# Kernel tuning notes

Hardware: AMD Instinct MI355X
Metric: run time of the kernel (lower is better)

## Reference

```python
import jax, jax.numpy as jnp
import numpy as np

B, L, D_MODEL = 2, 1024, 512
D_INNER, D_STATE, DT_RANK, D_CONV = 1024, 16, 32, 4
N_LAYER, VOCAB, EMBED_DIM, NUM_EMOTIONS = 2, 30000, 256, 7


def setup_inputs() -> dict:
    key = jax.random.key(0)
    ks = jax.random.split(key, 12)
    def n(k, shape, scale=0.02):
        return jax.random.normal(k, shape, jnp.float32) * scale
    A_init = jnp.broadcast_to(jnp.arange(1, D_STATE + 1, dtype=jnp.float32), (N_LAYER, D_INNER, D_STATE))
    return {
        "input_ids": jax.random.randint(ks[0], (B, L), 0, VOCAB),
        "embedding": n(ks[1], (VOCAB, D_MODEL)),
        "norm_w": jnp.ones((N_LAYER, D_MODEL)),
        "in_proj_w": n(ks[2], (N_LAYER, D_MODEL, 2 * D_INNER)),
        "conv_w": n(ks[3], (N_LAYER, D_INNER, 1, D_CONV), 0.1),
        "conv_b": jnp.zeros((N_LAYER, D_INNER)),
        "x_proj_w": n(ks[4], (N_LAYER, D_INNER, DT_RANK + 2 * D_STATE)),
        "dt_proj_w": n(ks[5], (N_LAYER, DT_RANK, D_INNER), 0.1),
        "dt_proj_b": jnp.zeros((N_LAYER, D_INNER)),
        "A_log": jnp.log(A_init),
        "D": jnp.ones((N_LAYER, D_INNER)),
        "out_proj_w": n(ks[6], (N_LAYER, D_INNER, D_MODEL)),
        "norm_f_w": jnp.ones((D_MODEL,)),
        "proj_w": n(ks[7], (D_MODEL, EMBED_DIM)),
        "proj_b": jnp.zeros((EMBED_DIM,)),
        "cls_w": n(ks[8], (EMBED_DIM, NUM_EMOTIONS)),
        "cls_b": jnp.zeros((NUM_EMOTIONS,)),
    }


def rmsnorm(x, w, eps=1e-5):
    return x * jax.lax.rsqrt(jnp.mean(x * x, axis=-1, keepdims=True) + eps) * w


def selective_scan(u, delta, A, B_, C, D_):
    # u, delta: [b,l,d]; A: [d,n]; B_, C: [b,l,n]; D_: [d]
    dA = jnp.exp(jnp.einsum('bld,dn->bldn', delta, A))          # [b,l,d,n]
    dBu = jnp.einsum('bld,bln,bld->bldn', delta, B_, u)          # [b,l,d,n]
    def step(h, inp):
        dA_t, dBu_t, C_t = inp                                   # [b,d,n],[b,d,n],[b,n]
        h = dA_t * h + dBu_t
        y = jnp.einsum('bdn,bn->bd', h, C_t)
        return h, y
    h0 = jnp.zeros((u.shape[0], u.shape[2], A.shape[1]), u.dtype)
    _, ys = jax.lax.scan(step, h0, (dA.transpose(1, 0, 2, 3), dBu.transpose(1, 0, 2, 3), C.transpose(1, 0, 2)))
    return ys.transpose(1, 0, 2) + u * D_                        # [b,l,d]


def mamba_block(x, in_w, cw, cb, xp_w, dt_w, dt_b, A_log, D_, out_w):
    # x: [b,l,d_model]
    xr = x @ in_w                                                # [b,l,2*d_inner]
    xi, res = jnp.split(xr, 2, axis=-1)
    # causal depthwise conv1d over time
    xc = jax.lax.conv_general_dilated(
        xi.transpose(0, 2, 1), cw, window_strides=(1,),
        padding=[(D_CONV - 1, 0)], feature_group_count=D_INNER,
        dimension_numbers=('NCH', 'OIH', 'NCH'))
    xi = jax.nn.silu(xc.transpose(0, 2, 1) + cb)                 # [b,l,d_inner]
    x_dbl = xi @ xp_w
    delta, B_, C = jnp.split(x_dbl, [DT_RANK, DT_RANK + D_STATE], axis=-1)
    delta = jax.nn.softplus(delta @ dt_w + dt_b)                 # [b,l,d_inner]
    A = -jnp.exp(A_log)
    y = selective_scan(xi, delta, A, B_, C, D_)
    y = y * jax.nn.silu(res)
    return y @ out_w                                             # [b,l,d_model]


def reference(input_ids, embedding, norm_w, in_proj_w, conv_w, conv_b, x_proj_w,
              dt_proj_w, dt_proj_b, A_log, D, out_proj_w, norm_f_w,
              proj_w, proj_b, cls_w, cls_b):
    x = embedding[input_ids]                                     # [b,l,d_model]
    for i in range(N_LAYER):
        x = x + mamba_block(rmsnorm(x, norm_w[i]), in_proj_w[i], conv_w[i],
                            conv_b[i], x_proj_w[i], dt_proj_w[i], dt_proj_b[i],
                            A_log[i], D[i], out_proj_w[i])
    x = rmsnorm(x, norm_f_w)
    pooled = x.mean(axis=1)                                      # [b,d_model]
    emotion_emb = pooled @ proj_w + proj_b                       # [b,embed_dim]
    logits = emotion_emb @ cls_w + cls_b                         # [b,num_emotions]
    return logits, emotion_emb
```

## Files before the change

kernel.cpp:

```cpp
#include <hip/hip_runtime.h>
#include <cstddef>

#define D_MODEL   512
#define D_INNER   1024
#define D_STATE   16
#define DT_RANK   32
#define SEQ_L     1024
#define BATCH     2
#define NLAYER    2
#define M_ROWS    (BATCH * SEQ_L)
#define NC        64
#define LC        (SEQ_L / NC)

typedef __bf16 bf16x8 __attribute__((ext_vector_type(8)));
typedef float  f32x4  __attribute__((ext_vector_type(4)));

__device__ __forceinline__ float softplus_f(float x) {
    return fmaxf(x, 0.f) + log1pf(expf(-fabsf(x)));
}
__device__ __forceinline__ float silu_f(float x) {
    return x / (1.f + __expf(-x));
}
__device__ __forceinline__ unsigned short f2bf(float f) {
    unsigned u = __float_as_uint(f);
    return (unsigned short)((u + 0x7fffu + ((u >> 16) & 1u)) >> 16);
}
__device__ __forceinline__ float bf2f(unsigned short v) {
    return __uint_as_float(((unsigned)v) << 16);
}
__device__ __forceinline__ unsigned pack_bf2(float lo, float hi) {
    return (unsigned)f2bf(lo) | ((unsigned)f2bf(hi) << 16);
}

__global__ __launch_bounds__(256) void init_kernel(const int* __restrict__ ids,
                                                   const float* __restrict__ emb,
                                                   const float* __restrict__ in_w,
                                                   const float* __restrict__ out_w,
                                                   float* __restrict__ x,
                                                   unsigned short* __restrict__ in_wt_all,
                                                   unsigned short* __restrict__ out_wt_all) {
    int z = blockIdx.z;
    if (z == 4) {
        int blk = blockIdx.y * 64 + blockIdx.x;
        if (blk >= 1024) return;
        int g = blk * 256 + threadIdx.x;
        int c = (g & 127) << 2;
        int m = g >> 7;
        int row = ids[m];
        *(float4*)&x[(size_t)m * D_MODEL + c] =
            *(const float4*)&emb[(size_t)row * D_MODEL + c];
        return;
    }
    const float* W; unsigned short* Wt; int K, N;
    if (z < 2) {
        if (blockIdx.x >= 64 || blockIdx.y >= 16) return;
        W = in_w + (size_t)z * 512 * 2048; Wt = in_wt_all + (size_t)z * 2048 * 512;
        K = 512; N = 2048;
    } else {
        int zz = z - 2;
        if (blockIdx.x >= 16 || blockIdx.y >= 32) return;
        W = out_w + (size_t)zz * 1024 * 512; Wt = out_wt_all + (size_t)zz * 512 * 1024;
        K = 1024; N = 512;
    }
    __shared__ float tile[32][33];
    int n0 = blockIdx.x * 32, k0 = blockIdx.y * 32;
    int tx = threadIdx.x & 31, ty = threadIdx.x >> 5;
    #pragma unroll
    for (int i = 0; i < 4; ++i)
        tile[ty + i*8][tx] = W[(size_t)(k0 + ty + i*8) * N + n0 + tx];
    __syncthreads();
    #pragma unroll
    for (int i = 0; i < 4; ++i)
        Wt[(size_t)(n0 + ty + i*8) * K + k0 + tx] = f2bf(tile[tx][ty + i*8]);
}

__global__ __launch_bounds__(64) void rmsnorm_bf_kernel(const float* __restrict__ x,
                                                        const float* __restrict__ w,
                                                        unsigned short* __restrict__ out) {
    int row = blockIdx.x;
    int tid = threadIdx.x;
    const float* xp = x + (size_t)row * D_MODEL;
    float4 v0 = *(const float4*)&xp[tid * 4];
    float4 v1 = *(const float4*)&xp[256 + tid * 4];
    float ss = v0.x*v0.x + v0.y*v0.y + v0.z*v0.z + v0.w*v0.w
             + v1.x*v1.x + v1.y*v1.y + v1.z*v1.z + v1.w*v1.w;
    #pragma unroll
    for (int off = 32; off > 0; off >>= 1) ss += __shfl_xor(ss, off);
    float scale = rsqrtf(ss * (1.f / D_MODEL) + 1e-5f);
    float4 w0 = *(const float4*)&w[tid * 4];
    float4 w1 = *(const float4*)&w[256 + tid * 4];
    unsigned short* op = out + (size_t)row * D_MODEL;
    uint2 p0, p1;
    p0.x = pack_bf2(v0.x * scale * w0.x, v0.y * scale * w0.y);
    p0.y = pack_bf2(v0.z * scale * w0.z, v0.w * scale * w0.w);
    p1.x = pack_bf2(v1.x * scale * w1.x, v1.y * scale * w1.y);
    p1.y = pack_bf2(v1.z * scale * w1.z, v1.w * scale * w1.w);
    *(uint2*)&op[tid * 4] = p0;
    *(uint2*)&op[256 + tid * 4] = p1;
}

template<int BMT, int BNT, int EPI>
__global__ __launch_bounds__(256) void gemm_mfma_t(const unsigned short* __restrict__ A,
                                                   const unsigned short* __restrict__ Bt,
                                                   float* __restrict__ C,
                                                   unsigned short* __restrict__ Cb,
                                                   int K, int ldc) {
    constexpr int FM = BMT / 32;
    constexpr int FN = BNT / 32;
    __shared__ unsigned short As[BMT * 64];
    __shared__ unsigned short Bs[BNT * 64];
    int m0 = blockIdx.y * BMT;
    int n0 = blockIdx.x * BNT;
    int t = threadIdx.x;
    int lane = t & 63, wave = t >> 6;
    int wr = wave >> 1, wc = wave & 1;
    int srow = t >> 3;
    int sc8  = t & 7;
    f32x4 acc[FM][FN] = {};

    for (int k0 = 0; k0 < K; k0 += 64) {
        __syncthreads();
        #pragma unroll
        for (int i = 0; i < BMT / 32; ++i) {
            int row = i * 32 + srow;
            int csrc = sc8 ^ (row & 7);
            __builtin_amdgcn_global_load_lds(
                (const __attribute__((address_space(1))) void*)
                    &A[(size_t)(m0 + row) * K + k0 + csrc * 8],
                (__attribute__((address_space(3))) void*)
                    &As[row * 64 + sc8 * 8], 16, 0, 0);
        }
        #pragma unroll
        for (int i = 0; i < BNT / 32; ++i) {
            int row = i * 32 + srow;
            int csrc = sc8 ^ (row & 7);
            __builtin_amdgcn_global_load_lds(
                (const __attribute__((address_space(1))) void*)
                    &Bt[(size_t)(n0 + row) * K + k0 + csrc * 8],
                (__attribute__((address_space(3))) void*)
                    &Bs[row * 64 + sc8 * 8], 16, 0, 0);
        }
        __syncthreads();
        #pragma unroll
        for (int ks = 0; ks < 2; ++ks) {
            bf16x8 av[FM], bv[FN];
            #pragma unroll
            for (int f = 0; f < FM; ++f) {
                int ar = wr * (FM * 16) + f * 16 + (lane & 15);
                int ac = (ks * 4 + (lane >> 4)) ^ (ar & 7);
                av[f] = *reinterpret_cast<const bf16x8*>(&As[ar * 64 + ac * 8]);
            }
            #pragma unroll
            for (int f = 0; f < FN; ++f) {
                int br = wc * (FN * 16) + f * 16 + (lane & 15);
                int bc = (ks * 4 + (lane >> 4)) ^ (br & 7);
                bv[f] = *reinterpret_cast<const bf16x8*>(&Bs[br * 64 + bc * 8]);
            }
            #pragma unroll
            for (int fm = 0; fm < FM; ++fm)
                #pragma unroll
                for (int fn = 0; fn < FN; ++fn)
                    acc[fm][fn] = __builtin_amdgcn_mfma_f32_16x16x32_bf16(
                        av[fm], bv[fn], acc[fm][fn], 0, 0, 0);
        }
    }
    #pragma unroll
    for (int fm = 0; fm < FM; ++fm)
        #pragma unroll
        for (int fn = 0; fn < FN; ++fn) {
            int row = m0 + wr * (FM * 16) + fm * 16 + (lane >> 4) * 4;
            int col = n0 + wc * (FN * 16) + fn * 16 + (lane & 15);
            #pragma unroll
            for (int r = 0; r < 4; ++r) {
                if (EPI == 2) C[(size_t)(row + r) * ldc + col] += acc[fm][fn][r];
                else          Cb[(size_t)(row + r) * ldc + col] = f2bf(acc[fm][fn][r]);
            }
        }
}

__global__ void conv_bf_kernel(const unsigned short* __restrict__ xi,
                               const float* __restrict__ cw,
                               const float* __restrict__ cb,
                               unsigned short* __restrict__ u) {
    int g = blockIdx.x * blockDim.x + threadIdx.x;
    int d = g & (D_INNER - 1);
    int m = g >> 10;
    int l = m & (SEQ_L - 1);
    float4 w = *(const float4*)&cw[d * 4];
    const unsigned short* col = &xi[(size_t)m * 2048 + d];
    float x3 = bf2f(col[0]);
    float x2 = (l >= 1) ? bf2f(col[-2048]) : 0.f;
    float x1 = (l >= 2) ? bf2f(col[-4096]) : 0.f;
    float x0 = (l >= 3) ? bf2f(col[-6144]) : 0.f;
    u[g] = f2bf(silu_f(cb[d] + w.x*x0 + w.y*x1 + w.z*x2 + w.w*x3));
}

__global__ __launch_bounds__(256) void xproj_kernel(const unsigned short* __restrict__ u,
                                                    const float* __restrict__ Bw,
                                                    float* __restrict__ Cc) {
    __shared__ float Bsh[64][68];
    __shared__ float Ash[4][64];
    int row0 = blockIdx.x * 4;
    int t = threadIdx.x;
    int tr = t >> 6, c = t & 63;
    int kk = t >> 2, cb4 = (t & 3) << 4;
    float acc = 0.f;
    for (int k0 = 0; k0 < 1024; k0 += 64) {
        __syncthreads();
        #pragma unroll
        for (int j = 0; j < 4; ++j) {
            float4 v = *(const float4*)&Bw[(size_t)(k0 + kk) * 64 + cb4 + j * 4];
            *(float4*)&Bsh[kk][cb4 + j * 4] = v;
        }
        Ash[tr][c] = bf2f(u[(size_t)(row0 + tr) * 1024 + k0 + c]);
        __syncthreads();
        #pragma unroll
        for (int k = 0; k < 64; ++k)
            acc = fmaf(Ash[tr][k], Bsh[k][c], acc);
    }
    Cc[(size_t)(row0 + tr) * 64 + c] = acc;
}

#define BM 64
#define BN 64
#define BKK 16
__global__ __launch_bounds__(256) void gemm_dt(const float* __restrict__ A,
                                               const float* __restrict__ Bm,
                                               const float* __restrict__ bias,
                                               float* __restrict__ C,
                                               int lda, int ldb, int ldc) {
    __shared__ float As[BM][BKK + 4];
    __shared__ float Bs[BKK][BN];
    int tid = threadIdx.x;
    int n0 = blockIdx.x * BN;
    int m0 = blockIdx.y * BM;
    int tx4 = (tid & 15) << 2;
    int ty4 = (tid >> 4) << 2;
    int arow = tid >> 2, akk = (tid & 3) << 2;
    int brow = tid >> 4, bcol = (tid & 15) << 2;
    float acc[4][4] = {};
    for (int k0 = 0; k0 < 32; k0 += BKK) {
        float4 av = *(const float4*)&A[(size_t)(m0 + arow) * lda + k0 + akk];
        float4 bv = *(const float4*)&Bm[(size_t)(k0 + brow) * ldb + n0 + bcol];
        *(float4*)&As[arow][akk] = av;
        *(float4*)&Bs[brow][bcol] = bv;
        __syncthreads();
        #pragma unroll
        for (int k = 0; k < BKK; ++k) {
            float a0 = As[ty4 + 0][k];
            float a1 = As[ty4 + 1][k];
            float a2 = As[ty4 + 2][k];
            float a3 = As[ty4 + 3][k];
            float4 b = *(float4*)&Bs[k][tx4];
            acc[0][0] = fmaf(a0, b.x, acc[0][0]); acc[0][1] = fmaf(a0, b.y, acc[0][1]);
            acc[0][2] = fmaf(a0, b.z, acc[0][2]); acc[0][3] = fmaf(a0, b.w, acc[0][3]);
            acc[1][0] = fmaf(a1, b.x, acc[1][0]); acc[1][1] = fmaf(a1, b.y, acc[1][1]);
            acc[1][2] = fmaf(a1, b.z, acc[1][2]); acc[1][3] = fmaf(a1, b.w, acc[1][3]);
            acc[2][0] = fmaf(a2, b.x, acc[2][0]); acc[2][1] = fmaf(a2, b.y, acc[2][1]);
            acc[2][2] = fmaf(a2, b.z, acc[2][2]); acc[2][3] = fmaf(a2, b.w, acc[2][3]);
            acc[3][0] = fmaf(a3, b.x, acc[3][0]); acc[3][1] = fmaf(a3, b.y, acc[3][1]);
            acc[3][2] = fmaf(a3, b.z, acc[3][2]); acc[3][3] = fmaf(a3, b.w, acc[3][3]);
        }
        __syncthreads();
    }
    #pragma unroll
    for (int i = 0; i < 4; ++i) {
        int m = m0 + ty4 + i;
        float4 bb = *(const float4*)&bias[n0 + tx4];
        float4 v = make_float4(softplus_f(acc[i][0] + bb.x), softplus_f(acc[i][1] + bb.y),
                               softplus_f(acc[i][2] + bb.z), softplus_f(acc[i][3] + bb.w));
        *(float4*)&C[(size_t)m * ldc + n0 + tx4] = v;
    }
}

__global__ __launch_bounds__(256) void scan_p1i(const unsigned short* __restrict__ u,
                                                const float* __restrict__ delta,
                                                const float* __restrict__ xdbl,
                                                const float* __restrict__ A_log,
                                                float* __restrict__ aprod,
                                                float* __restrict__ hloc) {
    int tid = threadIdx.x;
    int d = blockIdx.x * 256 + tid;
    int b = blockIdx.y, c = blockIdx.z;
    int l0 = c * LC;
    __shared__ float sBC[LC][32];
    for (int i = tid; i < LC * 32; i += 256) {
        int l = i >> 5, j = i & 31;
        sBC[l][j] = xdbl[(size_t)(b * SEQ_L + l0 + l) * 64 + 32 + j];
    }
    __syncthreads();
    float A_[D_STATE], h[D_STATE], ap[D_STATE];
    #pragma unroll
    for (int n = 0; n < D_STATE; ++n) {
        A_[n] = -__expf(A_log[(size_t)d * D_STATE + n]);
        h[n] = 0.f; ap[n] = 1.f;
    }
    const unsigned short* ucol = u + (size_t)(b * SEQ_L + l0) * D_INNER + d;
    const float* dcol = delta + (size_t)(b * SEQ_L + l0) * D_INNER + d;
    for (int l = 0; l < LC; ++l) {
        float dtv = dcol[l * D_INNER];
        float uu = bf2f(ucol[l * D_INNER]);
        float du = dtv * uu;
        #pragma unroll
        for (int n = 0; n < D_STATE; ++n) {
            float e = __expf(dtv * A_[n]);
            h[n] = fmaf(e, h[n], du * sBC[l][n]);
            ap[n] *= e;
        }
    }
    #pragma unroll
    for (int n = 0; n < D_STATE; ++n) {
        size_t o = (((size_t)b * NC + c) * D_STATE + n) * D_INNER + d;
        aprod[o] = ap[n];
        hloc[o] = h[n];
    }
}

__global__ __launch_bounds__(256) void scan_p2(const float* __restrict__ aprod,
                                               float* __restrict__ hloc) {
    int d = blockIdx.x * 256 + threadIdx.x;
    int n = blockIdx.y;
    int b = blockIdx.z;
    float h = 0.f;
    #pragma unroll 4
    for (int c = 0; c < NC; ++c) {
        size_t o = (((size_t)b * NC + c) * D_STATE + n) * D_INNER + d;
        float ap = aprod[o];
        float lc = hloc[o];
        hloc[o] = h;
        h = fmaf(ap, h, lc);
    }
}

__global__ __launch_bounds__(256) void scan_p3i(const unsigned short* __restrict__ u,
                                                const float* __restrict__ delta,
                                                const float* __restrict__ xdbl,
                                                const float* __restrict__ A_log,
                                                const float* __restrict__ Dp,
                                                const float* __restrict__ hinit,
                                                const unsigned short* __restrict__ xi,
                                                unsigned short* __restrict__ y) {
    int tid = threadIdx.x;
    int d = blockIdx.x * 256 + tid;
    int b = blockIdx.y, c = blockIdx.z;
    int l0 = c * LC;
    __shared__ float sBC[LC][32];
    for (int i = tid; i < LC * 32; i += 256) {
        int l = i >> 5, j = i & 31;
        sBC[l][j] = xdbl[(size_t)(b * SEQ_L + l0 + l) * 64 + 32 + j];
    }
    __syncthreads();
    float A_[D_STATE], h[D_STATE];
    #pragma unroll
    for (int n = 0; n < D_STATE; ++n) {
        A_[n] = -__expf(A_log[(size_t)d * D_STATE + n]);
        size_t o = (((size_t)b * NC + c) * D_STATE + n) * D_INNER + d;
        h[n] = hinit[o];
    }
    float Dd = Dp[d];
    const unsigned short* ucol = u  + (size_t)(b * SEQ_L + l0) * D_INNER + d;
    const float* dcol = delta + (size_t)(b * SEQ_L + l0) * D_INNER + d;
    const unsigned short* rcol = xi + (size_t)(b * SEQ_L + l0) * 2048 + 1024 + d;
    for (int l = 0; l < LC; ++l) {
        float dtv = dcol[l * D_INNER];
        float uu = bf2f(ucol[l * D_INNER]);
        float du = dtv * uu;
        float yv = 0.f;
        #pragma unroll
        for (int n = 0; n < D_STATE; ++n) {
            float e = __expf(dtv * A_[n]);
            h[n] = fmaf(e, h[n], du * sBC[l][n]);
            yv = fmaf(h[n], sBC[l][16 + n], yv);
        }
        yv = fmaf(uu, Dd, yv);
        float res = bf2f(rcol[l * 2048]);
        y[(size_t)(b * SEQ_L + l0 + l) * D_INNER + d] = f2bf(yv * silu_f(res));
    }
}

__global__ __launch_bounds__(256) void rms_pool1(const float* __restrict__ x,
                                                 float* __restrict__ partial) {
    int blk = blockIdx.x;
    int b = blk >> 5, c = blk & 31;
    int wave = threadIdx.x >> 6, lane = threadIdx.x & 63;
    int row0 = b * SEQ_L + c * 32 + wave * 8;
    float4 a0 = make_float4(0.f, 0.f, 0.f, 0.f);
    float4 a1 = make_float4(0.f, 0.f, 0.f, 0.f);
    for (int r = 0; r < 8; ++r) {
        const float* xp = x + (size_t)(row0 + r) * D_MODEL;
        float4 v0 = *(const float4*)&xp[lane * 4];
        float4 v1 = *(const float4*)&xp[256 + lane * 4];
        float ss = v0.x*v0.x + v0.y*v0.y + v0.z*v0.z + v0.w*v0.w
                 + v1.x*v1.x + v1.y*v1.y + v1.z*v1.z + v1.w*v1.w;
        #pragma unroll
        for (int off = 32; off > 0; off >>= 1) ss += __shfl_xor(ss, off);
        float s = rsqrtf(ss * (1.f / D_MODEL) + 1e-5f);
        a0.x = fmaf(v0.x, s, a0.x); a0.y = fmaf(v0.y, s, a0.y);
        a0.z = fmaf(v0.z, s, a0.z); a0.w = fmaf(v0.w, s, a0.w);
        a1.x = fmaf(v1.x, s, a1.x); a1.y = fmaf(v1.y, s, a1.y);
        a1.z = fmaf(v1.z, s, a1.z); a1.w = fmaf(v1.w, s, a1.w);
    }
    __shared__ float red[4][512];
    *(float4*)&red[wave][lane * 4] = a0;
    *(float4*)&red[wave][256 + lane * 4] = a1;
    __syncthreads();
    int d = threadIdx.x * 2;
    float s0 = red[0][d] + red[1][d] + red[2][d] + red[3][d];
    float s1 = red[0][d+1] + red[1][d+1] + red[2][d+1] + red[3][d+1];
    partial[(size_t)blk * 512 + d]     = s0;
    partial[(size_t)blk * 512 + d + 1] = s1;
}

__global__ __launch_bounds__(512) void tail2_kernel(const float* __restrict__ ppart,
                                                    const float* __restrict__ w,
                                                    const float* __restrict__ pw,
                                                    const float* __restrict__ pb,
                                                    const float* __restrict__ cw,
                                                    const float* __restrict__ cb,
                                                    float* __restrict__ out) {
    __shared__ float sp[2][512];
    __shared__ float se[2][256];
    int t = threadIdx.x;
    {
        int b = t >> 8, dp = (t & 255) * 2;
        float s0 = 0.f, s1 = 0.f;
        #pragma unroll 8
        for (int c = 0; c < 32; ++c) {
            const float* pp = &ppart[((size_t)b * 32 + c) * 512 + dp];
            s0 += pp[0]; s1 += pp[1];
        }
        sp[b][dp]     = s0 * (1.f / SEQ_L) * w[dp];
        sp[b][dp + 1] = s1 * (1.f / SEQ_L) * w[dp + 1];
    }
    __syncthreads();
    {
        int b = t >> 8, e = t & 255;
        float acc = pb[e];
        #pragma unroll 8
        for (int k = 0; k < 512; ++k)
            acc = fmaf(sp[b][k], pw[(size_t)k * 256 + e], acc);
        out[14 + b * 256 + e] = acc;
        se[b][e] = acc;
    }
    __syncthreads();
    {
        int wave = t >> 6, lane = t & 63;
        for (int idx = wave; idx < 14; idx += 8) {
            int bb = idx / 7, cc = idx % 7;
            float a = 0.f;
            #pragma unroll
            for (int i = 0; i < 4; ++i) {
                int k = lane + i * 64;
                a = fmaf(se[bb][k], cw[k * 7 + cc], a);
            }
            #pragma unroll
            for (int off = 32; off > 0; off >>= 1) a += __shfl_xor(a, off);
            if (lane == 0) out[bb * 7 + cc] = a + cb[cc];
        }
    }
}

extern "C" void kernel_launch(void* const* d_in, const int* in_sizes, int n_in,
                              void* d_out, int out_size, void* d_ws, size_t ws_size,
                              hipStream_t stream) {
    const int*   ids    = (const int*)d_in[0];
    const float* emb    = (const float*)d_in[1];
    const float* norm_w = (const float*)d_in[2];
    const float* in_w   = (const float*)d_in[3];
    const float* conv_w = (const float*)d_in[4];
    const float* conv_b = (const float*)d_in[5];
    const float* xp_w   = (const float*)d_in[6];
    const float* dt_w   = (const float*)d_in[7];
    const float* dt_b   = (const float*)d_in[8];
    const float* A_log  = (const float*)d_in[9];
    const float* Dp     = (const float*)d_in[10];
    const float* out_w  = (const float*)d_in[11];
    const float* normf  = (const float*)d_in[12];
    const float* proj_w = (const float*)d_in[13];
    const float* proj_b = (const float*)d_in[14];
    const float* cls_w  = (const float*)d_in[15];
    const float* cls_b  = (const float*)d_in[16];
    float* out = (float*)d_out;

    float* p = (float*)d_ws;
    float* x      = p; p += 1 << 20;
    float* xnr    = p; p += 1 << 20;
    float* xrr    = p; p += 2 << 20;
    float* urr    = p; p += 1 << 20;
    float* deltab = p; p += 2 << 20;
    float* xdbl   = p; p += 1 << 17;
    float* wreg   = p; p += 1572864;
    float* aprod  = p; p += 2 << 20;
    float* hloc   = p; p += 2 << 20;
    float* ybr    = p; p += 1 << 20;

    unsigned short* xn_bf  = (unsigned short*)xnr;
    float*          ppart  = xnr;
    unsigned short* xr_bf  = (unsigned short*)xrr;
    unsigned short* u_bf   = (unsigned short*)urr;
    unsigned short* in_wt_all  = (unsigned short*)wreg;
    unsigned short* out_wt_all = (unsigned short*)(wreg + (1 << 20));
    unsigned short* yb_bf  = (unsigned short*)ybr;

    init_kernel<<<dim3(64, 32, 5), 256, 0, stream>>>(
        ids, emb, in_w, out_w, x, in_wt_all, out_wt_all);

    for (int i = 0; i < NLAYER; ++i) {
        unsigned short* in_wt  = in_wt_all  + (size_t)i * 2048 * 512;
        unsigned short* out_wt = out_wt_all + (size_t)i * 512 * 1024;
        const float* cwi  = conv_w + (size_t)i * D_INNER * 4;
        const float* cbi  = conv_b + (size_t)i * D_INNER;
        const float* dtwi = dt_w + (size_t)i * DT_RANK * D_INNER;
        const float* dtbi = dt_b + (size_t)i * D_INNER;
        const float* Ali  = A_log + (size_t)i * D_INNER * D_STATE;
        const float* Dpi  = Dp + (size_t)i * D_INNER;

        rmsnorm_bf_kernel<<<M_ROWS, 64, 0, stream>>>(x, norm_w + i * D_MODEL, xn_bf);
        gemm_mfma_t<128, 64, 3><<<dim3(2048 / 64, M_ROWS / 128), 256, 0, stream>>>(
            xn_bf, in_wt, nullptr, xr_bf, 512, 2048);
        conv_bf_kernel<<<(M_ROWS * D_INNER) / 256, 256, 0, stream>>>(
            xr_bf, cwi, cbi, u_bf);
        xproj_kernel<<<M_ROWS / 4, 256, 0, stream>>>(
            u_bf, xp_w + (size_t)i * D_INNER * 64, xdbl);
        gemm_dt<<<dim3(1024 / BN, M_ROWS / BM), 256, 0, stream>>>(
            xdbl, dtwi, dtbi, deltab, 64, 1024, 1024);
        scan_p1i<<<dim3(4, BATCH, NC), 256, 0, stream>>>(
            u_bf, deltab, xdbl, Ali, aprod, hloc);
        scan_p2<<<dim3(4, D_STATE, BATCH), 256, 0, stream>>>(aprod, hloc);
        scan_p3i<<<dim3(4, BATCH, NC), 256, 0, stream>>>(
            u_bf, deltab, xdbl, Ali, Dpi, hloc, xr_bf, yb_bf);
        gemm_mfma_t<64, 32, 2><<<dim3(512 / 32, M_ROWS / 64), 256, 0, stream>>>(
            yb_bf, out_wt, x, nullptr, 1024, 512);
    }

    rms_pool1<<<BATCH * 32, 256, 0, stream>>>(x, ppart);
    tail2_kernel<<<1, 512, 0, stream>>>(ppart, normf, proj_w, proj_b, cls_w, cls_b, out);
}
```

Before: 244.5 us.

## Fuse first-layer RMSNorm into embedding gather and halve scan chunk count

The embedding gather in the init kernel now handles one row per wavefront, computes the row's RMS with a wave reduction, and writes the normalized bf16 activations directly. This removes the separate rmsnorm launch for layer 0. Separately, the number of scan chunks drops from 64 to 32, so each chunk is longer. That cuts the parallelism and the chunk-state traffic in the scan passes, and lengthens each chunk's serial work.

```diff
diff --git a/kernel.cpp b/kernel.cpp
--- a/kernel.cpp
+++ b/kernel.cpp
@@ -9,7 +9,7 @@
 #define BATCH     2
 #define NLAYER    2
 #define M_ROWS    (BATCH * SEQ_L)
-#define NC        64
+#define NC        32
 #define LC        (SEQ_L / NC)
 
 typedef __bf16 bf16x8 __attribute__((ext_vector_type(8)));
@@ -34,21 +34,41 @@
 
 __global__ __launch_bounds__(256) void init_kernel(const int* __restrict__ ids,
                                                    const float* __restrict__ emb,
+                                                   const float* __restrict__ nw0,
                                                    const float* __restrict__ in_w,
                                                    const float* __restrict__ out_w,
                                                    float* __restrict__ x,
+                                                   unsigned short* __restrict__ xn_bf,
                                                    unsigned short* __restrict__ in_wt_all,
                                                    unsigned short* __restrict__ out_wt_all) {
     int z = blockIdx.z;
     if (z == 4) {
         int blk = blockIdx.y * 64 + blockIdx.x;
-        if (blk >= 1024) return;
-        int g = blk * 256 + threadIdx.x;
-        int c = (g & 127) << 2;
-        int m = g >> 7;
+        if (blk >= 512) return;
+        int wave = threadIdx.x >> 6, lane = threadIdx.x & 63;
+        int m = blk * 4 + wave;
         int row = ids[m];
-        *(float4*)&x[(size_t)m * D_MODEL + c] =
-            *(const float4*)&emb[(size_t)row * D_MODEL + c];
+        const float* ep = emb + (size_t)row * D_MODEL;
+        float4 v0 = *(const float4*)&ep[lane * 4];
+        float4 v1 = *(const float4*)&ep[256 + lane * 4];
+        float* xp = x + (size_t)m * D_MODEL;
+        *(float4*)&xp[lane * 4] = v0;
+        *(float4*)&xp[256 + lane * 4] = v1;
+        float ss = v0.x*v0.x + v0.y*v0.y + v0.z*v0.z + v0.w*v0.w
+                 + v1.x*v1.x + v1.y*v1.y + v1.z*v1.z + v1.w*v1.w;
+        #pragma unroll
+        for (int off = 32; off > 0; off >>= 1) ss += __shfl_xor(ss, off);
+        float scale = rsqrtf(ss * (1.f / D_MODEL) + 1e-5f);
+        float4 w0 = *(const float4*)&nw0[lane * 4];
+        float4 w1 = *(const float4*)&nw0[256 + lane * 4];
+        unsigned short* op = xn_bf + (size_t)m * D_MODEL;
+        uint2 p0, p1;
+        p0.x = pack_bf2(v0.x * scale * w0.x, v0.y * scale * w0.y);
+        p0.y = pack_bf2(v0.z * scale * w0.z, v0.w * scale * w0.w);
+        p1.x = pack_bf2(v1.x * scale * w1.x, v1.y * scale * w1.y);
+        p1.y = pack_bf2(v1.z * scale * w1.z, v1.w * scale * w1.w);
+        *(uint2*)&op[lane * 4] = p0;
+        *(uint2*)&op[256 + lane * 4] = p1;
         return;
     }
     const float* W; unsigned short* Wt; int K, N;
@@ -503,7 +523,7 @@
     unsigned short* yb_bf  = (unsigned short*)ybr;
 
     init_kernel<<<dim3(64, 32, 5), 256, 0, stream>>>(
-        ids, emb, in_w, out_w, x, in_wt_all, out_wt_all);
+        ids, emb, norm_w, in_w, out_w, x, xn_bf, in_wt_all, out_wt_all);
 
     for (int i = 0; i < NLAYER; ++i) {
         unsigned short* in_wt  = in_wt_all  + (size_t)i * 2048 * 512;
@@ -515,7 +535,8 @@
         const float* Ali  = A_log + (size_t)i * D_INNER * D_STATE;
         const float* Dpi  = Dp + (size_t)i * D_INNER;
 
-        rmsnorm_bf_kernel<<<M_ROWS, 64, 0, stream>>>(x, norm_w + i * D_MODEL, xn_bf);
+        if (i > 0)
+            rmsnorm_bf_kernel<<<M_ROWS, 64, 0, stream>>>(x, norm_w + i * D_MODEL, xn_bf);
         gemm_mfma_t<128, 64, 3><<<dim3(2048 / 64, M_ROWS / 128), 256, 0, stream>>>(
             xn_bf, in_wt, nullptr, xr_bf, 512, 2048);
         conv_bf_kernel<<<(M_ROWS * D_INNER) / 256, 256, 0, stream>>>(
```

After: 258.4 us. +5.7%, slower.
